# Optimization experiments

Measured on AMD Instinct MI355X. Metric: run time of the kernel, lower is better.

The kernel has to match this reference:

```python
import jax, jax.numpy as jnp
import numpy as np

CMN_WINDOW = 600
MIN_CMN_WINDOW = 100
CENTER = False
NORM_VARS = True


def _window_bounds(num_frames, cmn_window, min_cmn_window, center):
    """Static (trace-time) per-frame window [start, end) exactly matching
    torchaudio.functional.sliding_window_cmn's boundary logic."""
    t = np.arange(num_frames)
    if center:
        ws = t - cmn_window // 2
        we = ws + cmn_window
    else:
        ws = t - cmn_window
        we = t + 1
    # if window_start < 0: shift right
    we = np.where(ws < 0, we - ws, we)
    ws = np.maximum(ws, 0)
    if not center:
        # if window_end > t: window_end = max(t+1, min_cmn_window)
        we = np.where(we > t, np.maximum(t + 1, min_cmn_window), we)
    # if window_end > num_frames: shift left, clamp
    ws = np.where(we > num_frames, ws - (we - num_frames), ws)
    we = np.minimum(we, num_frames)
    ws = np.maximum(ws, 0)
    return ws, we


def sliding_window_cmn(specgram, cmn_window, min_cmn_window, center, norm_vars):
    shape = specgram.shape
    num_frames, num_feats = shape[-2], shape[-1]
    x = specgram.reshape(-1, num_frames, num_feats)  # (B, T, F)
    B = x.shape[0]

    ws, we = _window_bounds(num_frames, cmn_window, min_cmn_window, center)
    n = jnp.asarray((we - ws), dtype=x.dtype)[None, :, None]  # (1, T, 1)

    zero = jnp.zeros((B, 1, num_feats), x.dtype)
    # exclusive prefix sums: cs[:, k] = sum of frames [0, k)
    cs = jnp.concatenate([zero, jnp.cumsum(x, axis=1)], axis=1)
    sums = jnp.take(cs, we, axis=1) - jnp.take(cs, ws, axis=1)  # (B, T, F)
    mean = sums / n
    out = x - mean

    if norm_vars:
        css = jnp.concatenate([zero, jnp.cumsum(x * x, axis=1)], axis=1)
        sumsq = jnp.take(css, we, axis=1) - jnp.take(css, ws, axis=1)
        variance = sumsq / n - mean * mean
        out = out * variance ** -0.5
        out = jnp.where(n == 1, jnp.zeros((), x.dtype), out)

    return out.reshape(shape)


def setup_inputs() -> dict:
    key = jax.random.key(0)
    specgram = jax.random.normal(key, (16, 60000, 80), dtype=jnp.float32)
    return {"specgram": specgram}


def reference(specgram):
    return sliding_window_cmn(specgram, CMN_WINDOW, MIN_CMN_WINDOW, CENTER, NORM_VARS)
```

## Files before the change

kernel.cpp:

```cpp
#include <hip/hip_runtime.h>

#define BN   16
#define TN   60000
#define FN   80
#define NF4  20
#define SEG  100
#define NSEG 600
#define WIN  600
#define SBK  6


__global__ __launch_bounds__(256) void k_segsum(const float* __restrict__ x,
                                                float* __restrict__ ck) {
    int tid = blockIdx.x * 256 + threadIdx.x;
    if (tid >= BN * NSEG * NF4) return;
    int f4   = tid % NF4;
    int seg  = (tid / NF4) % NSEG;
    int b    = tid / (NF4 * NSEG);
    const float* p = x + ((size_t)b * TN + (size_t)seg * SEG) * FN + f4 * 4;
    float s0=0.f,s1=0.f,s2=0.f,s3=0.f,q0=0.f,q1=0.f,q2=0.f,q3=0.f;
    for (int i = 0; i < SEG; ++i) {
        float4 v = *reinterpret_cast<const float4*>(p + (size_t)i * FN);
        s0 += v.x; s1 += v.y; s2 += v.z; s3 += v.w;
        q0 += v.x*v.x; q1 += v.y*v.y; q2 += v.z*v.z; q3 += v.w*v.w;
    }
    float* o = ck + (size_t)tid * 8;
    o[0]=s0; o[1]=s1; o[2]=s2; o[3]=s3;
    o[4]=q0; o[5]=q1; o[6]=q2; o[7]=q3;
}

__global__ __launch_bounds__(256) void k_out(const float* __restrict__ x,
                                             const float* __restrict__ ck,
                                             float* __restrict__ out) {
    int tid = blockIdx.x * 256 + threadIdx.x;
    if (tid >= BN * NSEG * NF4) return;
    int f4    = tid % NF4;
    int chunk = (tid / NF4) % NSEG;
    int b     = tid / (NF4 * NSEG);
    size_t base = ((size_t)b * TN + (size_t)chunk * SEG) * FN + f4 * 4;
    const float* xl = x + base;
    float* o = out + base;

    float ps0=0.f,ps1=0.f,ps2=0.f,ps3=0.f,pq0=0.f,pq1=0.f,pq2=0.f,pq3=0.f;
    {
        int start = chunk - SBK; if (start < 0) start = 0;
        const float* cp = ck + (((size_t)b * NSEG + start) * NF4 + f4) * 8;
        for (int j = start; j < chunk; ++j) {
            ps0 += cp[0]; ps1 += cp[1]; ps2 += cp[2]; ps3 += cp[3];
            pq0 += cp[4]; pq1 += cp[5]; pq2 += cp[6]; pq3 += cp[7];
            cp += NF4 * 8;
        }
    }

    if (chunk == 0) {
        const float* c0 = ck + (((size_t)b * NSEG) * NF4 + f4) * 8;
        const float rn = 1.0f / 100.0f;
        float m0=c0[0]*rn, m1=c0[1]*rn, m2=c0[2]*rn, m3=c0[3]*rn;
        float i0=rsqrtf(c0[4]*rn - m0*m0);
        float i1=rsqrtf(c0[5]*rn - m1*m1);
        float i2=rsqrtf(c0[6]*rn - m2*m2);
        float i3=rsqrtf(c0[7]*rn - m3*m3);
        for (int i = 0; i < SEG; ++i) {
            float4 v = *reinterpret_cast<const float4*>(xl + (size_t)i * FN);
            float4 r;
            r.x = (v.x - m0) * i0; r.y = (v.y - m1) * i1;
            r.z = (v.z - m2) * i2; r.w = (v.w - m3) * i3;
            *reinterpret_cast<float4*>(o + (size_t)i * FN) = r;
        }
    } else if (chunk < SBK) {
        float ls0=ps0, ls1=ps1, ls2=ps2, ls3=ps3;
        float lq0=pq0, lq1=pq1, lq2=pq2, lq3=pq3;
        for (int i = 0; i < SEG; ++i) {
            float4 v = *reinterpret_cast<const float4*>(xl + (size_t)i * FN);
            ls0 += v.x; ls1 += v.y; ls2 += v.z; ls3 += v.w;
            lq0 += v.x*v.x; lq1 += v.y*v.y; lq2 += v.z*v.z; lq3 += v.w*v.w;
            float rn = 1.0f / (float)(chunk * SEG + i + 1);
            float m0=ls0*rn, m1=ls1*rn, m2=ls2*rn, m3=ls3*rn;
            float4 r;
            r.x = (v.x - m0) * rsqrtf(lq0*rn - m0*m0);
            r.y = (v.y - m1) * rsqrtf(lq1*rn - m1*m1);
            r.z = (v.z - m2) * rsqrtf(lq2*rn - m2*m2);
            r.w = (v.w - m3) * rsqrtf(lq3*rn - m3*m3);
            *reinterpret_cast<float4*>(o + (size_t)i * FN) = r;
        }
    } else {
        float ls0=ps0, ls1=ps1, ls2=ps2, ls3=ps3;
        float lq0=pq0, lq1=pq1, lq2=pq2, lq3=pq3;
        float ts0=0.f, ts1=0.f, ts2=0.f, ts3=0.f;
        float tq0=0.f, tq1=0.f, tq2=0.f, tq3=0.f;
        const float* xt = xl - (size_t)WIN * FN;
        const float rn = 1.0f / 601.0f;
        for (int i = 0; i < SEG; ++i) {
            float4 v = *reinterpret_cast<const float4*>(xl + (size_t)i * FN);
            float4 w = *reinterpret_cast<const float4*>(xt + (size_t)i * FN);
            ls0 += v.x; ls1 += v.y; ls2 += v.z; ls3 += v.w;
            lq0 += v.x*v.x; lq1 += v.y*v.y; lq2 += v.z*v.z; lq3 += v.w*v.w;
            float s0 = ls0 - ts0, s1 = ls1 - ts1, s2 = ls2 - ts2, s3 = ls3 - ts3;
            float q0 = lq0 - tq0, q1 = lq1 - tq1, q2 = lq2 - tq2, q3 = lq3 - tq3;
            float m0 = s0*rn, m1 = s1*rn, m2 = s2*rn, m3 = s3*rn;
            float4 r;
            r.x = (v.x - m0) * rsqrtf(q0*rn - m0*m0);
            r.y = (v.y - m1) * rsqrtf(q1*rn - m1*m1);
            r.z = (v.z - m2) * rsqrtf(q2*rn - m2*m2);
            r.w = (v.w - m3) * rsqrtf(q3*rn - m3*m3);
            *reinterpret_cast<float4*>(o + (size_t)i * FN) = r;
            ts0 += w.x; ts1 += w.y; ts2 += w.z; ts3 += w.w;
            tq0 += w.x*w.x; tq1 += w.y*w.y; tq2 += w.z*w.z; tq3 += w.w*w.w;
        }
    }
}

extern "C" void kernel_launch(void* const* d_in, const int* in_sizes, int n_in,
                              void* d_out, int out_size, void* d_ws, size_t ws_size,
                              hipStream_t stream) {
    const float* x = (const float*)d_in[0];
    float* out = (float*)d_out;
    float* ck = (float*)d_ws;

    const int n1 = BN * NSEG * NF4;
    k_segsum<<<(n1 + 255) / 256, 256, 0, stream>>>(x, ck);
    k_out<<<(n1 + 255) / 256, 256, 0, stream>>>(x, ck, out);
}
```

Measured before the change: 610.4 us.

## Fuse segment-sum pass into CMN kernel by directly summing 600-frame window prefix

Removes the separate segment-sum kernel and workspace. Each thread now reads the 600 frames preceding its chunk to seed its running window sums, then slides the window by subtracting the leaving frame instead of keeping separate tail accumulators. This drops a kernel launch and the workspace write and read, but each thread now reads about 600 extra frames, roughly seven times the earlier per-thread input traffic, though much of it may hit cache. Running subtraction over a long sum may also add floating-point drift.

```diff
diff --git a/kernel.cpp b/kernel.cpp
--- a/kernel.cpp
+++ b/kernel.cpp
@@ -10,27 +10,7 @@
 #define SBK  6
 
 
-__global__ __launch_bounds__(256) void k_segsum(const float* __restrict__ x,
-                                                float* __restrict__ ck) {
-    int tid = blockIdx.x * 256 + threadIdx.x;
-    if (tid >= BN * NSEG * NF4) return;
-    int f4   = tid % NF4;
-    int seg  = (tid / NF4) % NSEG;
-    int b    = tid / (NF4 * NSEG);
-    const float* p = x + ((size_t)b * TN + (size_t)seg * SEG) * FN + f4 * 4;
-    float s0=0.f,s1=0.f,s2=0.f,s3=0.f,q0=0.f,q1=0.f,q2=0.f,q3=0.f;
-    for (int i = 0; i < SEG; ++i) {
-        float4 v = *reinterpret_cast<const float4*>(p + (size_t)i * FN);
-        s0 += v.x; s1 += v.y; s2 += v.z; s3 += v.w;
-        q0 += v.x*v.x; q1 += v.y*v.y; q2 += v.z*v.z; q3 += v.w*v.w;
-    }
-    float* o = ck + (size_t)tid * 8;
-    o[0]=s0; o[1]=s1; o[2]=s2; o[3]=s3;
-    o[4]=q0; o[5]=q1; o[6]=q2; o[7]=q3;
-}
-
-__global__ __launch_bounds__(256) void k_out(const float* __restrict__ x,
-                                             const float* __restrict__ ck,
+__global__ __launch_bounds__(256) void k_cmn(const float* __restrict__ x,
                                              float* __restrict__ out) {
     int tid = blockIdx.x * 256 + threadIdx.x;
     if (tid >= BN * NSEG * NF4) return;
@@ -41,25 +21,20 @@
     const float* xl = x + base;
     float* o = out + base;
 
-    float ps0=0.f,ps1=0.f,ps2=0.f,ps3=0.f,pq0=0.f,pq1=0.f,pq2=0.f,pq3=0.f;
-    {
-        int start = chunk - SBK; if (start < 0) start = 0;
-        const float* cp = ck + (((size_t)b * NSEG + start) * NF4 + f4) * 8;
-        for (int j = start; j < chunk; ++j) {
-            ps0 += cp[0]; ps1 += cp[1]; ps2 += cp[2]; ps3 += cp[3];
-            pq0 += cp[4]; pq1 += cp[5]; pq2 += cp[6]; pq3 += cp[7];
-            cp += NF4 * 8;
-        }
-    }
+    float ls0=0.f,ls1=0.f,ls2=0.f,ls3=0.f,lq0=0.f,lq1=0.f,lq2=0.f,lq3=0.f;
 
     if (chunk == 0) {
-        const float* c0 = ck + (((size_t)b * NSEG) * NF4 + f4) * 8;
+        for (int i = 0; i < SEG; ++i) {
+            float4 v = *reinterpret_cast<const float4*>(xl + (size_t)i * FN);
+            ls0 += v.x; ls1 += v.y; ls2 += v.z; ls3 += v.w;
+            lq0 += v.x*v.x; lq1 += v.y*v.y; lq2 += v.z*v.z; lq3 += v.w*v.w;
+        }
         const float rn = 1.0f / 100.0f;
-        float m0=c0[0]*rn, m1=c0[1]*rn, m2=c0[2]*rn, m3=c0[3]*rn;
-        float i0=rsqrtf(c0[4]*rn - m0*m0);
-        float i1=rsqrtf(c0[5]*rn - m1*m1);
-        float i2=rsqrtf(c0[6]*rn - m2*m2);
-        float i3=rsqrtf(c0[7]*rn - m3*m3);
+        float m0=ls0*rn, m1=ls1*rn, m2=ls2*rn, m3=ls3*rn;
+        float i0=rsqrtf(lq0*rn - m0*m0);
+        float i1=rsqrtf(lq1*rn - m1*m1);
+        float i2=rsqrtf(lq2*rn - m2*m2);
+        float i3=rsqrtf(lq3*rn - m3*m3);
         for (int i = 0; i < SEG; ++i) {
             float4 v = *reinterpret_cast<const float4*>(xl + (size_t)i * FN);
             float4 r;
@@ -67,9 +42,20 @@
             r.z = (v.z - m2) * i2; r.w = (v.w - m3) * i3;
             *reinterpret_cast<float4*>(o + (size_t)i * FN) = r;
         }
-    } else if (chunk < SBK) {
-        float ls0=ps0, ls1=ps1, ls2=ps2, ls3=ps3;
-        float lq0=pq0, lq1=pq1, lq2=pq2, lq3=pq3;
+        return;
+    }
+
+    const int initN = (chunk >= SBK) ? WIN : chunk * SEG;
+    {
+        const float* ip = xl - (size_t)initN * FN;
+        for (int i = 0; i < initN; ++i) {
+            float4 v = *reinterpret_cast<const float4*>(ip + (size_t)i * FN);
+            ls0 += v.x; ls1 += v.y; ls2 += v.z; ls3 += v.w;
+            lq0 += v.x*v.x; lq1 += v.y*v.y; lq2 += v.z*v.z; lq3 += v.w*v.w;
+        }
+    }
+
+    if (chunk < SBK) {
         for (int i = 0; i < SEG; ++i) {
             float4 v = *reinterpret_cast<const float4*>(xl + (size_t)i * FN);
             ls0 += v.x; ls1 += v.y; ls2 += v.z; ls3 += v.w;
@@ -84,10 +70,6 @@
             *reinterpret_cast<float4*>(o + (size_t)i * FN) = r;
         }
     } else {
-        float ls0=ps0, ls1=ps1, ls2=ps2, ls3=ps3;
-        float lq0=pq0, lq1=pq1, lq2=pq2, lq3=pq3;
-        float ts0=0.f, ts1=0.f, ts2=0.f, ts3=0.f;
-        float tq0=0.f, tq1=0.f, tq2=0.f, tq3=0.f;
         const float* xt = xl - (size_t)WIN * FN;
         const float rn = 1.0f / 601.0f;
         for (int i = 0; i < SEG; ++i) {
@@ -95,17 +77,15 @@
             float4 w = *reinterpret_cast<const float4*>(xt + (size_t)i * FN);
             ls0 += v.x; ls1 += v.y; ls2 += v.z; ls3 += v.w;
             lq0 += v.x*v.x; lq1 += v.y*v.y; lq2 += v.z*v.z; lq3 += v.w*v.w;
-            float s0 = ls0 - ts0, s1 = ls1 - ts1, s2 = ls2 - ts2, s3 = ls3 - ts3;
-            float q0 = lq0 - tq0, q1 = lq1 - tq1, q2 = lq2 - tq2, q3 = lq3 - tq3;
-            float m0 = s0*rn, m1 = s1*rn, m2 = s2*rn, m3 = s3*rn;
+            float m0=ls0*rn, m1=ls1*rn, m2=ls2*rn, m3=ls3*rn;
             float4 r;
-            r.x = (v.x - m0) * rsqrtf(q0*rn - m0*m0);
-            r.y = (v.y - m1) * rsqrtf(q1*rn - m1*m1);
-            r.z = (v.z - m2) * rsqrtf(q2*rn - m2*m2);
-            r.w = (v.w - m3) * rsqrtf(q3*rn - m3*m3);
+            r.x = (v.x - m0) * rsqrtf(lq0*rn - m0*m0);
+            r.y = (v.y - m1) * rsqrtf(lq1*rn - m1*m1);
+            r.z = (v.z - m2) * rsqrtf(lq2*rn - m2*m2);
+            r.w = (v.w - m3) * rsqrtf(lq3*rn - m3*m3);
             *reinterpret_cast<float4*>(o + (size_t)i * FN) = r;
-            ts0 += w.x; ts1 += w.y; ts2 += w.z; ts3 += w.w;
-            tq0 += w.x*w.x; tq1 += w.y*w.y; tq2 += w.z*w.z; tq3 += w.w*w.w;
+            ls0 -= w.x; ls1 -= w.y; ls2 -= w.z; ls3 -= w.w;
+            lq0 -= w.x*w.x; lq1 -= w.y*w.y; lq2 -= w.z*w.z; lq3 -= w.w*w.w;
         }
     }
 }
@@ -115,9 +95,8 @@
                               hipStream_t stream) {
     const float* x = (const float*)d_in[0];
     float* out = (float*)d_out;
-    float* ck = (float*)d_ws;
+    (void)d_ws; (void)ws_size;
 
     const int n1 = BN * NSEG * NF4;
-    k_segsum<<<(n1 + 255) / 256, 256, 0, stream>>>(x, ck);
-    k_out<<<(n1 + 255) / 256, 256, 0, stream>>>(x, ck, out);
+    k_cmn<<<(n1 + 255) / 256, 256, 0, stream>>>(x, out);
 }
```

New measurement: 910.1 us. 1.49x slower.
